# Kernel optimization log

Hardware: AMD Instinct MI355X
Metric: run time of the kernel (lower is better)

## Reference

```python
import jax, jax.numpy as jnp
import numpy as np

N = 100000
E = 1600000
D_IN = 128
H = 128


def _param(key, shape, scale=0.05):
    return jax.random.normal(key, shape, dtype=jnp.float32) * scale


def setup_inputs() -> dict:
    key = jax.random.key(0)
    ks = jax.random.split(key, 24)
    inp = {
        'x': jax.random.normal(ks[0], (N, D_IN), dtype=jnp.float32),
        'edge_index': jax.random.randint(ks[1], (2, E), 0, N, dtype=jnp.int64),
        'h1': jax.random.normal(ks[2], (N, H), dtype=jnp.float32),
        'h2': jax.random.normal(ks[3], (N, H), dtype=jnp.float32),
        'h3': jax.random.normal(ks[4], (N, H), dtype=jnp.float32),
        # GCNConv params (PyG: lin weight applied as x @ W, W: [in, out] here)
        'gcn1_w': _param(ks[5], (D_IN, H)),
        'gcn1_b': jnp.zeros((H,), jnp.float32),
        'gcn2_w': _param(ks[6], (H, H)),
        'gcn2_b': jnp.zeros((H,), jnp.float32),
    }
    # torch.nn.GRUCell params: weight_ih [3H, in], weight_hh [3H, H], biases [3H]
    for i, kw in zip((1, 2, 3), (ks[7], ks[10], ks[13])):
        k1, k2, k3 = jax.random.split(kw, 3)
        inp[f'gru{i}_wih'] = _param(k1, (3 * H, H))
        inp[f'gru{i}_whh'] = _param(k2, (3 * H, H))
        inp[f'gru{i}_bih'] = _param(k3, (3 * H,))
        inp[f'gru{i}_bhh'] = jnp.zeros((3 * H,), jnp.float32)
    return inp


def gcn_conv(x, src, dst, w, b):
    """PyG GCNConv: D^-1/2 (A+I) D^-1/2 X W + b (symmetric norm, self-loops)."""
    xw = x @ w  # [N, H]
    ones = jnp.ones((src.shape[0],), xw.dtype)
    # degree including self-loop
    deg = jax.ops.segment_sum(ones, dst, num_segments=N) + 1.0
    dinv = jax.lax.rsqrt(deg)
    norm = dinv[src] * dinv[dst]  # [E]
    agg = jax.ops.segment_sum(xw[src] * norm[:, None], dst, num_segments=N)
    # self-loop contribution: norm = dinv[i]*dinv[i] = 1/deg[i]
    return agg + xw / deg[:, None] + b


def gru_cell(x, h, w_ih, w_hh, b_ih, b_hh):
    gi = x @ w_ih.T + b_ih  # [N, 3H]
    gh = h @ w_hh.T + b_hh
    i_r, i_z, i_n = jnp.split(gi, 3, axis=-1)
    h_r, h_z, h_n = jnp.split(gh, 3, axis=-1)
    r = jax.nn.sigmoid(i_r + h_r)
    z = jax.nn.sigmoid(i_z + h_z)
    n = jnp.tanh(i_n + r * h_n)
    return (1.0 - z) * n + z * h


def reference(x, edge_index, h1, h2, h3,
              gcn1_w, gcn1_b, gcn2_w, gcn2_b,
              gru1_wih, gru1_whh, gru1_bih, gru1_bhh,
              gru2_wih, gru2_whh, gru2_bih, gru2_bhh,
              gru3_wih, gru3_whh, gru3_bih, gru3_bhh):
    src, dst = edge_index[0], edge_index[1]
    x = jax.nn.relu(gcn_conv(x, src, dst, gcn1_w, gcn1_b))
    # dropout is identity at eval
    x = jax.nn.relu(gcn_conv(x, src, dst, gcn2_w, gcn2_b))
    h1n = gru_cell(x, h1, gru1_wih, gru1_whh, gru1_bih, gru1_bhh)
    h2n = gru_cell(h1n, h2, gru2_wih, gru2_whh, gru2_bih, gru2_bhh)
    h3n = gru_cell(h2n, h3, gru3_wih, gru3_whh, gru3_bih, gru3_bhh)
    return (h1n, h2n, h3n)
```

## Files before the change

### kernel.cpp

```cpp
#include <hip/hip_runtime.h>
#include <hip/hip_bf16.h>

#define DH 128
#define SCB 1024
#define NCHUNK 256

typedef __attribute__((ext_vector_type(8))) short short8_t;
typedef __attribute__((ext_vector_type(4))) float f32x4;

static __device__ __forceinline__ short f2bf(float f) {
    union { float f; unsigned u; } v; v.f = f;
    unsigned r = v.u + 0x7fffu + ((v.u >> 16) & 1u);
    return (short)(r >> 16);
}

static __device__ __forceinline__ float bf2f(unsigned short b) {
    union { unsigned u; float f; } v; v.u = ((unsigned)b) << 16;
    return v.f;
}

static __device__ __forceinline__ short8_t cvt8(const float* p) {
    float4 a0 = *(const float4*)p;
    float4 a1 = *(const float4*)(p + 4);
    short8_t t;
    t[0] = f2bf(a0.x); t[1] = f2bf(a0.y); t[2] = f2bf(a0.z); t[3] = f2bf(a0.w);
    t[4] = f2bf(a1.x); t[5] = f2bf(a1.y); t[6] = f2bf(a1.z); t[7] = f2bf(a1.w);
    return t;
}

static __device__ __forceinline__ float sigm(float x) {
    return __builtin_amdgcn_rcpf(1.f + __expf(-x));
}
static __device__ __forceinline__ float tanh_f(float x) {
    return 1.f - 2.f * __builtin_amdgcn_rcpf(__expf(2.f * x) + 1.f);
}

__global__ __launch_bounds__(256) void deg2_k(const int* __restrict__ ei, int E,
                                              unsigned* __restrict__ cnt, int span, int chunkE) {
    int r = blockIdx.x & 7;
    int c = blockIdx.x >> 3;
    int lo = r * span, hi = lo + span;
    long long e0 = (long long)c * chunkE;
    long long e1 = e0 + chunkE; if (e1 > E) e1 = E;
    for (long long e = e0 + threadIdx.x; e < e1; e += 256) {
        int d = ei[E + e];
        if (d >= lo && d < hi) atomicAdd(&cnt[d], 1u);
    }
}

__global__ __launch_bounds__(256) void scan1_k(const unsigned* __restrict__ cnt, int N,
                                               int* __restrict__ offs, unsigned* __restrict__ bsum) {
    __shared__ unsigned s[256];
    int t = threadIdx.x;
    int i0 = blockIdx.x * SCB + t * 4;
    unsigned v0 = (i0 + 0 < N) ? cnt[i0 + 0] : 0u;
    unsigned v1 = (i0 + 1 < N) ? cnt[i0 + 1] : 0u;
    unsigned v2 = (i0 + 2 < N) ? cnt[i0 + 2] : 0u;
    unsigned v3 = (i0 + 3 < N) ? cnt[i0 + 3] : 0u;
    unsigned ts = v0 + v1 + v2 + v3;
    s[t] = ts;
    __syncthreads();
    for (int off = 1; off < 256; off <<= 1) {
        unsigned u = (t >= off) ? s[t - off] : 0u;
        __syncthreads();
        s[t] += u;
        __syncthreads();
    }
    unsigned ex = s[t] - ts;
    if (i0 + 0 < N) offs[i0 + 0] = (int)ex;
    if (i0 + 1 < N) offs[i0 + 1] = (int)(ex + v0);
    if (i0 + 2 < N) offs[i0 + 2] = (int)(ex + v0 + v1);
    if (i0 + 3 < N) offs[i0 + 3] = (int)(ex + v0 + v1 + v2);
    if (t == 255) bsum[blockIdx.x] = s[255];
}

__global__ __launch_bounds__(1024) void scan2_k(unsigned* __restrict__ bsum, int B) {
    __shared__ unsigned s[1024];
    int t = threadIdx.x;
    unsigned v = (t < B) ? bsum[t] : 0u;
    s[t] = v;
    __syncthreads();
    for (int off = 1; off < 1024; off <<= 1) {
        unsigned u = (t >= off) ? s[t - off] : 0u;
        __syncthreads();
        s[t] += u;
        __syncthreads();
    }
    if (t < B) bsum[t] = s[t] - v;
    if (t == 0) bsum[B] = s[1023];
}

__global__ void scan3_k(int* __restrict__ offs, int* __restrict__ cur,
                        float* __restrict__ dinv, const unsigned* __restrict__ cnt,
                        const unsigned* __restrict__ bsum, int N, int B) {
    int i = blockIdx.x * 256 + threadIdx.x;
    if (i < N) {
        int v = offs[i] + (int)bsum[i >> 10];
        offs[i] = v;
        cur[i] = v;
        dinv[i] = rsqrtf((float)cnt[i] + 1.0f);
    }
    if (i == 0) offs[N] = (int)bsum[B];
}

__global__ __launch_bounds__(256) void fill2_k(const int* __restrict__ ei, int E,
                                               int* __restrict__ cur, int* __restrict__ csr_src,
                                               int span, int chunkE) {
    int r = blockIdx.x & 7;
    int c = blockIdx.x >> 3;
    int lo = r * span, hi = lo + span;
    long long e0 = (long long)c * chunkE;
    long long e1 = e0 + chunkE; if (e1 > E) e1 = E;
    for (long long e = e0 + threadIdx.x; e < e1; e += 256) {
        int d = ei[E + e];
        if (d >= lo && d < hi) {
            int pos = atomicAdd(&cur[d], 1);
            csr_src[pos] = ei[e];
        }
    }
}

__global__ void f2bf6_k(const float* __restrict__ s0, const float* __restrict__ s1,
                        const float* __restrict__ s2, const float* __restrict__ s3,
                        const float* __restrict__ s4, const float* __restrict__ s5,
                        short* __restrict__ dst, int WN) {
    int i = blockIdx.x * 256 + threadIdx.x;
    if (i >= 6 * WN) return;
    int b = i / WN, r = i - b * WN;
    const float* srcs[6] = {s0, s1, s2, s3, s4, s5};
    dst[i] = f2bf(srcs[b][r]);
}

__global__ void transpose_bf2_k(const float* __restrict__ sa, const float* __restrict__ sb,
                                short* __restrict__ da, short* __restrict__ db) {
    int i = blockIdx.x * 256 + threadIdx.x;
    int m = i >> 14;
    int j = i & 16383;
    int c = j >> 7, k = j & 127;
    const float* s = m ? sb : sa;
    short* d = m ? db : da;
    d[j] = f2bf(s[k * DH + c]);
}

__global__ __launch_bounds__(256, 4) void gemm_mfma_k(const float* __restrict__ A,
                                                      const short* __restrict__ Wt,
                                                      const float* __restrict__ dinv,
                                                      short* __restrict__ C, int N) {
    int tid = threadIdx.x;
    int wave = tid >> 6, lane = tid & 63;
    int lr = lane & 15, kg = lane >> 4;

    int row0 = blockIdx.x * 128 + wave * 32;
    int ar0 = min(row0 + lr, N - 1);
    int ar1 = min(row0 + 16 + lr, N - 1);
    const float* a0p = A + (size_t)ar0 * DH;
    const float* a1p = A + (size_t)ar1 * DH;
    short8_t af[2][4];
#pragma unroll
    for (int ks = 0; ks < 4; ks++) {
        af[0][ks] = cvt8(a0p + ks * 32 + kg * 8);
        af[1][ks] = cvt8(a1p + ks * 32 + kg * 8);
    }

    float di0[4], di1[4];
#pragma unroll
    for (int j = 0; j < 4; j++) {
        di0[j] = dinv[min(row0 + kg * 4 + j, N - 1)];
        di1[j] = dinv[min(row0 + 16 + kg * 4 + j, N - 1)];
    }

    short8_t bt[3][4];
#define GLOADW(slot, t) { \
    const short* wp = Wt + (size_t)((t) * 16 + lr) * DH + kg * 8; \
    bt[slot][0] = *(const short8_t*)(wp); \
    bt[slot][1] = *(const short8_t*)(wp + 32); \
    bt[slot][2] = *(const short8_t*)(wp + 64); \
    bt[slot][3] = *(const short8_t*)(wp + 96); }

    GLOADW(0, 0)
    GLOADW(1, 1)
#pragma unroll
    for (int t = 0; t < 8; t++) {
        if (t < 6) GLOADW((t + 2) % 3, t + 2)
        f32x4 acc0 = {0.f, 0.f, 0.f, 0.f};
        f32x4 acc1 = {0.f, 0.f, 0.f, 0.f};
#pragma unroll
        for (int ks = 0; ks < 4; ks++) {
            acc0 = __builtin_amdgcn_mfma_f32_16x16x32_bf16(af[0][ks], bt[t % 3][ks], acc0, 0, 0, 0);
            acc1 = __builtin_amdgcn_mfma_f32_16x16x32_bf16(af[1][ks], bt[t % 3][ks], acc1, 0, 0, 0);
        }
        int col = t * 16 + lr;
#pragma unroll
        for (int j = 0; j < 4; j++) {
            int g0 = row0 + kg * 4 + j;
            int g1 = row0 + 16 + kg * 4 + j;
            if (g0 < N) C[(size_t)g0 * DH + col] = f2bf(acc0[j] * di0[j]);
            if (g1 < N) C[(size_t)g1 * DH + col] = f2bf(acc1[j] * di1[j]);
        }
    }
#undef GLOADW
}

__global__ __launch_bounds__(256) void gather_k(const int* __restrict__ csr_src,
                                                const int* __restrict__ offs,
                                                const float* __restrict__ dinv,
                                                const unsigned* __restrict__ xws,
                                                const float* __restrict__ bias,
                                                float* __restrict__ dest, int N) {
    int wid = blockIdx.x * 4 + (threadIdx.x >> 6);
    if (wid >= N) return;
    int lane = threadIdx.x & 63;
    int j = offs[wid];
    int end = offs[wid + 1];
    float dd = dinv[wid];

    unsigned xv = xws[(size_t)wid * 64 + lane];
    float ax = bf2f((unsigned short)(xv & 0xffffu));
    float ay = bf2f((unsigned short)(xv >> 16));

#define ACC(w) { ax += bf2f((unsigned short)((w) & 0xffffu)); \
                 ay += bf2f((unsigned short)((w) >> 16)); }

    if (j + 4 <= end) {
        int a0 = csr_src[j], a1 = csr_src[j + 1], a2 = csr_src[j + 2], a3 = csr_src[j + 3];
        j += 4;
        for (; j + 4 <= end; j += 4) {
            unsigned w0 = xws[(size_t)a0 * 64 + lane];
            unsigned w1 = xws[(size_t)a1 * 64 + lane];
            unsigned w2 = xws[(size_t)a2 * 64 + lane];
            unsigned w3 = xws[(size_t)a3 * 64 + lane];
            a0 = csr_src[j]; a1 = csr_src[j + 1]; a2 = csr_src[j + 2]; a3 = csr_src[j + 3];
            ACC(w0) ACC(w1) ACC(w2) ACC(w3)
        }
        unsigned w0 = xws[(size_t)a0 * 64 + lane];
        unsigned w1 = xws[(size_t)a1 * 64 + lane];
        unsigned w2 = xws[(size_t)a2 * 64 + lane];
        unsigned w3 = xws[(size_t)a3 * 64 + lane];
        ACC(w0) ACC(w1) ACC(w2) ACC(w3)
    }
    for (; j < end; ++j) {
        unsigned w = xws[(size_t)csr_src[j] * 64 + lane];
        ACC(w)
    }
#undef ACC

    float2 b2 = ((const float2*)bias)[lane];
    float ox = fmaxf(fmaf(dd, ax, b2.x), 0.f);
    float oy = fmaxf(fmaf(dd, ay, b2.y), 0.f);
    float2 o; o.x = ox; o.y = oy;
    ((float2*)dest)[(size_t)wid * 64 + lane] = o;
}

__global__ __launch_bounds__(512, 1) void gru3_mfma_k(
        const float* __restrict__ X, const float* __restrict__ H1,
        const float* __restrict__ H2, const float* __restrict__ H3,
        const short* __restrict__ w1i, const short* __restrict__ w1h,
        const short* __restrict__ w2i, const short* __restrict__ w2h,
        const short* __restrict__ w3i, const short* __restrict__ w3h,
        const float* __restrict__ bi1, const float* __restrict__ bh1,
        const float* __restrict__ bi2, const float* __restrict__ bh2,
        const float* __restrict__ bi3, const float* __restrict__ bh3,
        float* __restrict__ o1, float* __restrict__ o2, float* __restrict__ o3,
        int N) {
    __shared__ short lds[2][64 * DH];
    int tid = threadIdx.x;
    int row0 = blockIdx.x * 64;
    int wave = tid >> 6, lane = tid & 63;
    int lr = lane & 15, kg = lane >> 4;
    int c0 = wave * 16;

    const short* wihs[3] = {w1i, w2i, w3i};
    const short* whhs[3] = {w1h, w2h, w3h};
    const float* bihs[3] = {bi1, bi2, bi3};
    const float* bhhs[3] = {bh1, bh2, bh3};
    const float* hnexts[2] = {H2, H3};
    float* outs[3] = {o1, o2, o3};

    short8_t bw[3][4], bu[3][4];
#define WLOADALL(wih_, whh_) { \
    _Pragma("unroll") \
    for (int g = 0; g < 3; g++) { \
        const short* wi = (wih_) + (size_t)(g * DH + c0 + lr) * DH + kg * 8; \
        const short* wh = (whh_) + (size_t)(g * DH + c0 + lr) * DH + kg * 8; \
        _Pragma("unroll") \
        for (int ks = 0; ks < 4; ks++) { \
            bw[g][ks] = *(const short8_t*)(wi + ks * 32); \
            bu[g][ks] = *(const short8_t*)(wh + ks * 32); \
        } \
    } }

    WLOADALL(w1i, w1h)

    {
        int mat = tid >> 8;
        int r = (tid & 255) >> 2;
        int q = tid & 3;
        int grow = min(row0 + r, N - 1);
        const float* src = (mat ? H1 : X) + (size_t)grow * DH + q * 32;
        char* dst = (char*)&lds[mat][r * DH];
#pragma unroll
        for (int j = 0; j < 4; j++) {
            short8_t v = cvt8(src + j * 8);
            int boff = (q * 64 + j * 16) ^ ((r & 7) << 4);
            *(short8_t*)(dst + boff) = v;
        }
    }
    __syncthreads();

    int gcol = c0 + lr;
    int colb = gcol * 2;

#pragma unroll
    for (int cell = 0; cell < 3; cell++) {
        f32x4 aR[4], aZ[4], aI[4], aH[4];
#pragma unroll
        for (int rt = 0; rt < 4; rt++) {
            aR[rt] = (f32x4){0,0,0,0}; aZ[rt] = (f32x4){0,0,0,0};
            aI[rt] = (f32x4){0,0,0,0}; aH[rt] = (f32x4){0,0,0,0};
        }
#pragma unroll
        for (int rt = 0; rt < 4; rt++) {
            int r = rt * 16 + lr;
            char* xrow = (char*)&lds[0][r * DH];
            char* hrow = (char*)&lds[1][r * DH];
            short8_t xa[4], ha[4];
#pragma unroll
            for (int ks = 0; ks < 4; ks++) {
                int boff = (ks * 64 + kg * 16) ^ ((r & 7) << 4);
                xa[ks] = *(short8_t*)(xrow + boff);
                ha[ks] = *(short8_t*)(hrow + boff);
            }
#pragma unroll
            for (int ks = 0; ks < 4; ks++) {
                aR[rt] = __builtin_amdgcn_mfma_f32_16x16x32_bf16(xa[ks], bw[0][ks], aR[rt], 0, 0, 0);
                aR[rt] = __builtin_amdgcn_mfma_f32_16x16x32_bf16(ha[ks], bu[0][ks], aR[rt], 0, 0, 0);
                aZ[rt] = __builtin_amdgcn_mfma_f32_16x16x32_bf16(xa[ks], bw[1][ks], aZ[rt], 0, 0, 0);
                aZ[rt] = __builtin_amdgcn_mfma_f32_16x16x32_bf16(ha[ks], bu[1][ks], aZ[rt], 0, 0, 0);
                aI[rt] = __builtin_amdgcn_mfma_f32_16x16x32_bf16(xa[ks], bw[2][ks], aI[rt], 0, 0, 0);
                aH[rt] = __builtin_amdgcn_mfma_f32_16x16x32_bf16(ha[ks], bu[2][ks], aH[rt], 0, 0, 0);
            }
        }

        const float* bih = bihs[cell];
        const float* bhh = bhhs[cell];
        float br = bih[gcol], bz = bih[DH + gcol], bn = bih[2 * DH + gcol];
        float cr = bhh[gcol], cz = bhh[DH + gcol], cn = bhh[2 * DH + gcol];
        float* outp = outs[cell];
        short hb[4][4];
#pragma unroll
        for (int rt = 0; rt < 4; rt++) {
#pragma unroll
            for (int j = 0; j < 4; j++) {
                int r = rt * 16 + kg * 4 + j;
                float hv = bf2f(*(unsigned short*)((char*)&lds[1][r * DH] + (colb ^ ((r & 7) << 4))));
                float rr = sigm(aR[rt][j] + br + cr);
                float zz = sigm(aZ[rt][j] + bz + cz);
                float nn = tanh_f(aI[rt][j] + bn + rr * (aH[rt][j] + cn));
                float ov = (1.f - zz) * nn + zz * hv;
                int grow = row0 + r;
                if (grow < N) outp[(size_t)grow * DH + gcol] = ov;
                hb[rt][j] = f2bf(ov);
            }
        }

        if (cell < 2) {
            WLOADALL(wihs[cell + 1], whhs[cell + 1])
        }

        __syncthreads();

        if (cell < 2) {
#pragma unroll
            for (int rt = 0; rt < 4; rt++) {
#pragma unroll
                for (int j = 0; j < 4; j++) {
                    int r = rt * 16 + kg * 4 + j;
                    *(short*)((char*)&lds[0][r * DH] + (colb ^ ((r & 7) << 4))) = hb[rt][j];
                }
            }
            {
                int r = tid >> 3;
                int q = tid & 7;
                int grow = min(row0 + r, N - 1);
                const float* src = hnexts[cell] + (size_t)grow * DH + q * 16;
                char* dst = (char*)&lds[1][r * DH];
#pragma unroll
                for (int j = 0; j < 2; j++) {
                    short8_t v = cvt8(src + j * 8);
                    int boff = (q * 32 + j * 16) ^ ((r & 7) << 4);
                    *(short8_t*)(dst + boff) = v;
                }
            }
            __syncthreads();
        }
    }
#undef WLOADALL
}

extern "C" void kernel_launch(void* const* d_in, const int* in_sizes, int n_in,
                              void* d_out, int out_size, void* d_ws, size_t ws_size,
                              hipStream_t stream) {
    const float* x    = (const float*)d_in[0];
    const int*   ei   = (const int*)d_in[1];
    const float* h1   = (const float*)d_in[2];
    const float* h2   = (const float*)d_in[3];
    const float* h3   = (const float*)d_in[4];
    const float* g1w  = (const float*)d_in[5];
    const float* g1b  = (const float*)d_in[6];
    const float* g2w  = (const float*)d_in[7];
    const float* g2b  = (const float*)d_in[8];
    const float* wih1 = (const float*)d_in[9];
    const float* whh1 = (const float*)d_in[10];
    const float* bih1 = (const float*)d_in[11];
    const float* bhh1 = (const float*)d_in[12];
    const float* wih2 = (const float*)d_in[13];
    const float* whh2 = (const float*)d_in[14];
    const float* bih2 = (const float*)d_in[15];
    const float* bhh2 = (const float*)d_in[16];
    const float* wih3 = (const float*)d_in[17];
    const float* whh3 = (const float*)d_in[18];
    const float* bih3 = (const float*)d_in[19];
    const float* bhh3 = (const float*)d_in[20];

    int N = in_sizes[0] / DH;
    int E = in_sizes[1] / 2;
    int B = (N + SCB - 1) / SCB;
    int nstripes = (N + 127) / 128;
    int nblk64 = (N + 63) / 64;
    int span = (N + 7) / 8;
    int chunkE = (E + NCHUNK - 1) / NCHUNK;

    char* wsp = (char*)d_ws;
    auto alloc = [&](size_t bytes) -> char* {
        char* p = wsp;
        wsp += (bytes + 63) & ~(size_t)63;
        return p;
    };
    unsigned* cnt = (unsigned*)alloc((size_t)N * 4);
    int* offs     = (int*)alloc(((size_t)N + 1) * 4);
    int* cur      = (int*)alloc((size_t)N * 4);
    float* dinv   = (float*)alloc((size_t)N * 4);
    unsigned* bsum= (unsigned*)alloc(((size_t)B + 1) * 4);
    int* csr_src  = (int*)alloc((size_t)E * 4);
    short* xwb    = (short*)alloc((size_t)N * DH * 2);
    float* x2     = (float*)alloc((size_t)N * DH * 4);
    short* w1t    = (short*)alloc((size_t)DH * DH * 2);
    short* w2t    = (short*)alloc((size_t)DH * DH * 2);
    const int WN = 3 * DH * DH;
    short* wbAll  = (short*)alloc((size_t)6 * WN * 2);
    short* wb[6];
    for (int i = 0; i < 6; i++) wb[i] = wbAll + (size_t)i * WN;

    float* out  = (float*)d_out;
    float* h1n  = out;
    float* h2n  = out + (size_t)N * DH;
    float* h3n  = out + 2 * (size_t)N * DH;

    f2bf6_k<<<(6 * WN + 255) / 256, 256, 0, stream>>>(wih1, whh1, wih2, whh2, wih3, whh3, wbAll, WN);
    transpose_bf2_k<<<(2 * DH * DH + 255) / 256, 256, 0, stream>>>(g1w, g2w, w1t, w2t);

    hipMemsetAsync(cnt, 0, (size_t)N * 4, stream);
    deg2_k<<<8 * NCHUNK, 256, 0, stream>>>(ei, E, cnt, span, chunkE);
    scan1_k<<<B, 256, 0, stream>>>(cnt, N, offs, bsum);
    scan2_k<<<1, 1024, 0, stream>>>(bsum, B);
    scan3_k<<<(N + 255) / 256, 256, 0, stream>>>(offs, cur, dinv, cnt, bsum, N, B);
    fill2_k<<<8 * NCHUNK, 256, 0, stream>>>(ei, E, cur, csr_src, span, chunkE);

    int gblocks = (N + 3) / 4;

    gemm_mfma_k<<<nstripes, 256, 0, stream>>>(x, w1t, dinv, xwb, N);
    gather_k<<<gblocks, 256, 0, stream>>>(csr_src, offs, dinv, (const unsigned*)xwb, g1b, x2, N);

    gemm_mfma_k<<<nstripes, 256, 0, stream>>>(x2, w2t, dinv, xwb, N);
    gather_k<<<gblocks, 256, 0, stream>>>(csr_src, offs, dinv, (const unsigned*)xwb, g2b, x2, N);

    gru3_mfma_k<<<nblk64, 512, 0, stream>>>(x2, h1, h2, h3,
                                            wb[0], wb[1], wb[2], wb[3], wb[4], wb[5],
                                            bih1, bhh1, bih2, bhh2, bih3, bhh3,
                                            h1n, h2n, h3n, N);
}
```

Baseline: 575.5 us.

## Preload all GRU hidden states into padded LDS upfront and raise occupancy hint

The fused three-cell GRU kernel now stages X, H1, H2 and H3 into four padded LDS slots at kernel start, before the weight load. This replaces the per-cell reload of the next hidden state that sat between barriers. The XOR swizzle is dropped in favour of a 136-element row pitch to avoid bank conflicts. Launch bounds change from 1 to 4 blocks per CU to let the compiler budget registers for more resident blocks, at the cost of roughly doubled LDS per block and possible register pressure on the large weight fragments.

```diff
diff --git a/kernel.cpp b/kernel.cpp
--- a/kernel.cpp
+++ b/kernel.cpp
@@ -4,6 +4,7 @@
 #define DH 128
 #define SCB 1024
 #define NCHUNK 256
+#define LROW 136
 
 typedef __attribute__((ext_vector_type(8))) short short8_t;
 typedef __attribute__((ext_vector_type(4))) float f32x4;
@@ -251,7 +252,7 @@
     ((float2*)dest)[(size_t)wid * 64 + lane] = o;
 }
 
-__global__ __launch_bounds__(512, 1) void gru3_mfma_k(
+__global__ __launch_bounds__(512, 4) void gru3_mfma_k(
         const float* __restrict__ X, const float* __restrict__ H1,
         const float* __restrict__ H2, const float* __restrict__ H3,
         const short* __restrict__ w1i, const short* __restrict__ w1h,
@@ -262,7 +263,7 @@
         const float* __restrict__ bi3, const float* __restrict__ bh3,
         float* __restrict__ o1, float* __restrict__ o2, float* __restrict__ o3,
         int N) {
-    __shared__ short lds[2][64 * DH];
+    __shared__ short lds[4][64 * LROW];
     int tid = threadIdx.x;
     int row0 = blockIdx.x * 64;
     int wave = tid >> 6, lane = tid & 63;
@@ -273,7 +274,6 @@
     const short* whhs[3] = {w1h, w2h, w3h};
     const float* bihs[3] = {bi1, bi2, bi3};
     const float* bhhs[3] = {bh1, bh2, bh3};
-    const float* hnexts[2] = {H2, H3};
     float* outs[3] = {o1, o2, o3};
 
     short8_t bw[3][4], bu[3][4];
@@ -289,22 +289,21 @@
         } \
     } }
 
+    {
+        const float* mats[4] = {X, H1, H2, H3};
+        int mat = tid >> 7;
+        int rr = (tid & 127) >> 1;
+        int q = tid & 1;
+        int grow = min(row0 + rr, N - 1);
+        const float* src = mats[mat] + (size_t)grow * DH + q * 64;
+        char* dst = (char*)&lds[mat][rr * LROW] + q * 128;
+#pragma unroll
+        for (int j = 0; j < 8; j++) {
+            short8_t v = cvt8(src + j * 8);
+            *(short8_t*)(dst + j * 16) = v;
+        }
+    }
     WLOADALL(w1i, w1h)
-
-    {
-        int mat = tid >> 8;
-        int r = (tid & 255) >> 2;
-        int q = tid & 3;
-        int grow = min(row0 + r, N - 1);
-        const float* src = (mat ? H1 : X) + (size_t)grow * DH + q * 32;
-        char* dst = (char*)&lds[mat][r * DH];
-#pragma unroll
-        for (int j = 0; j < 4; j++) {
-            short8_t v = cvt8(src + j * 8);
-            int boff = (q * 64 + j * 16) ^ ((r & 7) << 4);
-            *(short8_t*)(dst + boff) = v;
-        }
-    }
     __syncthreads();
 
     int gcol = c0 + lr;
@@ -312,6 +311,7 @@
 
 #pragma unroll
     for (int cell = 0; cell < 3; cell++) {
+        const short* hslot = lds[cell + 1];
         f32x4 aR[4], aZ[4], aI[4], aH[4];
 #pragma unroll
         for (int rt = 0; rt < 4; rt++) {
@@ -321,14 +321,14 @@
 #pragma unroll
         for (int rt = 0; rt < 4; rt++) {
             int r = rt * 16 + lr;
-            char* xrow = (char*)&lds[0][r * DH];
-            char* hrow = (char*)&lds[1][r * DH];
+            const char* xrow = (const char*)&lds[0][r * LROW];
+            const char* hrow = (const char*)&hslot[r * LROW];
             short8_t xa[4], ha[4];
 #pragma unroll
             for (int ks = 0; ks < 4; ks++) {
-                int boff = (ks * 64 + kg * 16) ^ ((r & 7) << 4);
-                xa[ks] = *(short8_t*)(xrow + boff);
-                ha[ks] = *(short8_t*)(hrow + boff);
+                int boff = ks * 64 + kg * 16;
+                xa[ks] = *(const short8_t*)(xrow + boff);
+                ha[ks] = *(const short8_t*)(hrow + boff);
             }
 #pragma unroll
             for (int ks = 0; ks < 4; ks++) {
@@ -352,7 +352,7 @@
 #pragma unroll
             for (int j = 0; j < 4; j++) {
                 int r = rt * 16 + kg * 4 + j;
-                float hv = bf2f(*(unsigned short*)((char*)&lds[1][r * DH] + (colb ^ ((r & 7) << 4))));
+                float hv = bf2f(*(const unsigned short*)((const char*)&hslot[r * LROW] + colb));
                 float rr = sigm(aR[rt][j] + br + cr);
                 float zz = sigm(aZ[rt][j] + bz + cz);
                 float nn = tanh_f(aI[rt][j] + bn + rr * (aH[rt][j] + cn));
@@ -375,20 +375,7 @@
 #pragma unroll
                 for (int j = 0; j < 4; j++) {
                     int r = rt * 16 + kg * 4 + j;
-                    *(short*)((char*)&lds[0][r * DH] + (colb ^ ((r & 7) << 4))) = hb[rt][j];
-                }
-            }
-            {
-                int r = tid >> 3;
-                int q = tid & 7;
-                int grow = min(row0 + r, N - 1);
-                const float* src = hnexts[cell] + (size_t)grow * DH + q * 16;
-                char* dst = (char*)&lds[1][r * DH];
-#pragma unroll
-                for (int j = 0; j < 2; j++) {
-                    short8_t v = cvt8(src + j * 8);
-                    int boff = (q * 32 + j * 16) ^ ((r & 7) << 4);
-                    *(short8_t*)(dst + boff) = v;
+                    *(short*)((char*)&lds[0][r * LROW] + colb) = hb[rt][j];
                 }
             }
             __syncthreads();
```

Measured after the change: 712.1 us. +23.7%, slower.
